# Optimization experiments

Hardware: AMD Instinct MI355X
Metric: run time of the kernel (lower is better)

Reference implementation:

```python
import jax, jax.numpy as jnp
import numpy as np
from jax import lax

B, H, W, C = 2, 256, 256, 192
HEADS = 6
WS = 8                      # window size
PW = WS // 2                # permuted window size (kv downsampled 2x2)
HIDDEN = 4 * C
HEAD_DIM = C // HEADS
SCALE = HEAD_DIM ** -0.5
N_WIN = WS * WS             # 64 query tokens per window
N_KV = PW * PW              # 16 kv tokens per window


def _aligned_index(pw0, pw1):
    ch = np.arange(pw0)
    cw = np.arange(pw1)
    coords = np.stack(np.meshgrid(ch, cw, indexing='ij'))          # (2, pw0, pw1)
    cf = coords.reshape(2, -1)
    rel = (cf[:, :, None] - cf[:, None, :]).transpose(1, 2, 0).astype(np.int64)
    rel[:, :, 0] += pw0 - 1
    rel[:, :, 1] += pw1 - 1
    rel[:, :, 0] *= 2 * pw1 - 1
    idx = rel.sum(-1)                                              # (N_KV, N_KV)
    n4 = pw0 * pw1
    idx = idx.reshape(pw0, pw1, 1, 1, n4)
    idx = np.tile(idx, (1, 1, 2, 2, 1)).transpose(0, 2, 1, 3, 4).reshape(4 * n4, n4)
    return jnp.asarray(idx)

IDX = _aligned_index(PW, PW)   # (N_WIN, N_KV)


def layernorm(x, g, b):
    mu = x.mean(-1, keepdims=True)
    var = ((x - mu) ** 2).mean(-1, keepdims=True)
    return (x - mu) * lax.rsqrt(var + 1e-5) * g + b


def window_partition(x):
    # (B, H, W, C) -> (B*nW, WS, WS, C)
    x = x.reshape(B, H // WS, WS, W // WS, WS, C)
    return x.transpose(0, 1, 3, 2, 4, 5).reshape(-1, WS, WS, C)


def window_reverse(w):
    # (B*nW, WS, WS, C) -> (B, H, W, C)
    x = w.reshape(B, H // WS, W // WS, WS, WS, C)
    return x.transpose(0, 1, 3, 2, 4, 5).reshape(B, H, W, C)


def setup_inputs() -> dict:
    key = jax.random.key(0)
    ks = jax.random.split(key, 10)
    rn = lambda k, shp, s=0.02: jax.random.normal(k, shp, jnp.float32) * s
    return {
        'x': jax.random.normal(ks[0], (B, H * W, C), jnp.float32),
        'g1': jnp.ones((C,), jnp.float32), 'be1': jnp.zeros((C,), jnp.float32),
        'wq': rn(ks[1], (C, C)), 'bq': jnp.zeros((C,), jnp.float32),
        'wkv': rn(ks[2], (C, C // 2)), 'bkv': jnp.zeros((C // 2,), jnp.float32),
        'bias_table': rn(ks[3], ((2 * PW - 1) * (2 * PW - 1), HEADS)),
        'wproj': rn(ks[4], (C, C)), 'bproj': jnp.zeros((C,), jnp.float32),
        'g2': jnp.ones((C,), jnp.float32), 'be2': jnp.zeros((C,), jnp.float32),
        'w1f': rn(ks[5], (C, HIDDEN)), 'b1f': jnp.zeros((HIDDEN,), jnp.float32),
        'dwk': rn(ks[6], (HIDDEN, 1, 5, 5)), 'dwb': jnp.zeros((HIDDEN,), jnp.float32),
        'w2f': rn(ks[7], (HIDDEN, C)), 'b2f': jnp.zeros((C,), jnp.float32),
    }


def reference(x, g1, be1, wq, bq, wkv, bkv, bias_table, wproj, bproj,
              g2, be2, w1f, b1f, dwk, dwb, w2f, b2f):
    shortcut = x
    xn = layernorm(x, g1, be1).reshape(B, H, W, C)
    xw = window_partition(xn).reshape(-1, N_WIN, C)        # (b_, 64, C)
    b_ = xw.shape[0]
    # PSA: kv downsampled 2x2 spatially, 2x2 block folded into channels
    kv = (xw @ wkv + bkv).reshape(b_, PW, 2, PW, 2, 2, C // 4)
    kv = kv.transpose(0, 1, 3, 5, 2, 4, 6).reshape(b_, N_KV, 2, HEADS, HEAD_DIM)
    kv = kv.transpose(2, 0, 3, 1, 4)                       # (2, b_, h, N_KV, d)
    k, v = kv[0], kv[1]
    q = (xw @ wq + bq).reshape(b_, N_WIN, HEADS, HEAD_DIM).transpose(0, 2, 1, 3) * SCALE
    attn = jnp.einsum('bhqd,bhkd->bhqk', q, k)             # (b_, h, 64, 16)
    bias = bias_table[IDX.reshape(-1)].reshape(N_WIN, N_KV, HEADS).transpose(2, 0, 1)
    attn = jax.nn.softmax(attn + bias[None], axis=-1)
    aw = jnp.einsum('bhqk,bhkd->bhqd', attn, v).transpose(0, 2, 1, 3).reshape(b_, N_WIN, C)
    aw = aw @ wproj + bproj
    x = shortcut + window_reverse(aw.reshape(-1, WS, WS, C)).reshape(B, H * W, C)
    # ConvFFN with depthwise-conv residual branch
    xn2 = layernorm(x, g2, be2)
    h1 = jax.nn.gelu(xn2 @ w1f + b1f, approximate=False)   # (B, HW, HIDDEN)
    img = h1.transpose(0, 2, 1).reshape(B, HIDDEN, H, W)
    conv = lax.conv_general_dilated(img, dwk, (1, 1), ((2, 2), (2, 2)),
                                    feature_group_count=HIDDEN,
                                    dimension_numbers=('NCHW', 'OIHW', 'NCHW'))
    conv = jax.nn.gelu(conv + dwb[None, :, None, None], approximate=False)
    h = h1 + conv.reshape(B, HIDDEN, H * W).transpose(0, 2, 1)
    return x + (h @ w2f + b2f)
```

## Files before the change

### kernel.cpp

```cpp
#include <hip/hip_runtime.h>
#include <hip/hip_bf16.h>
#include <math.h>

#define NTOK  131072
#define NTOKH 65536
#define CD    192
#define HID   768


typedef short bf16x8 __attribute__((ext_vector_type(8)));
typedef float f32x4  __attribute__((ext_vector_type(4)));
typedef float f32x2  __attribute__((ext_vector_type(2)));
typedef __bf16 bf16x2_t __attribute__((ext_vector_type(2)));

__device__ __forceinline__ float bf2f(unsigned short v) {
    union { unsigned int u; float f; } c; c.u = ((unsigned int)v) << 16; return c.f;
}
__device__ __forceinline__ unsigned short f2bf(float f) {
    union { float f; unsigned int u; } c; c.f = f;
    unsigned int r = c.u + 0x7FFFu + ((c.u >> 16) & 1u);
    return (unsigned short)(r >> 16);
}
__device__ __forceinline__ float lo_bf(unsigned p) {
    union { unsigned u; float f; } c; c.u = p << 16; return c.f;
}
__device__ __forceinline__ float hi_bf(unsigned p) {
    union { unsigned u; float f; } c; c.u = p & 0xFFFF0000u; return c.f;
}
__device__ __forceinline__ float dot2bf(unsigned a, unsigned b, float c) {
#if __has_builtin(__builtin_amdgcn_fdot2_f32_bf16)
    union U { unsigned u; bf16x2_t v; };
    U ua, ub; ua.u = a; ub.u = b;
    return __builtin_amdgcn_fdot2_f32_bf16(ua.v, ub.v, c, false);
#else
    return fmaf(hi_bf(a) , hi_bf(b), fmaf(lo_bf(a), lo_bf(b), c));
#endif
}
__device__ __forceinline__ float gelu_f(float x) {
    float t = x * 0.7071067811865476f;
    t = fminf(fmaxf(t, -4.0f), 4.0f);
    float s2 = t * t;
    float p = fmaf(s2, -2.72614225801306e-10f, 2.77068142495902e-08f);
    p = fmaf(s2, p, -2.10102402082508e-06f);
    p = fmaf(s2, p, -5.69250639462346e-05f);
    p = fmaf(s2, p, -7.34990630326855e-04f);
    p = fmaf(s2, p, -2.95459980854025e-03f);
    p = fmaf(s2, p, -1.60960333262415e-02f);
    p = p * t;
    float q = fmaf(s2, -1.45660718464996e-05f, -2.13374055278905e-04f);
    q = fmaf(s2, q, -1.68282697438203e-03f);
    q = fmaf(s2, q, -7.37332916720468e-03f);
    q = fmaf(s2, q, -1.42647390514189e-02f);
    float er = p * __builtin_amdgcn_rcpf(q);
    return 0.5f * x * (1.0f + er);
}

__device__ __forceinline__ void gld16(const unsigned short* g, unsigned short* l) {
    __builtin_amdgcn_global_load_lds(
        (const __attribute__((address_space(1))) void*)(unsigned long long)(g),
        (__attribute__((address_space(3))) void*)(unsigned int)(unsigned long long)(l),
        16, 0, 0);
}

__global__ __launch_bounds__(256) void ln_kernel(const float* __restrict__ x,
                                                 const float* __restrict__ g,
                                                 const float* __restrict__ b,
                                                 unsigned short* __restrict__ out) {
    int tok  = blockIdx.x * 4 + (threadIdx.x >> 6);
    int lane = threadIdx.x & 63;
    const float* xp = x + (size_t)tok * CD;
    float v0 = xp[lane], v1 = xp[lane + 64], v2 = xp[lane + 128];
    float s  = v0 + v1 + v2;
    float s2 = v0 * v0 + v1 * v1 + v2 * v2;
    #pragma unroll
    for (int off = 32; off > 0; off >>= 1) {
        s  += __shfl_xor(s,  off, 64);
        s2 += __shfl_xor(s2, off, 64);
    }
    float mu  = s * (1.0f / 192.0f);
    float var = s2 * (1.0f / 192.0f) - mu * mu;
    float rs  = rsqrtf(var + 1e-5f);
    unsigned short* op = out + (size_t)tok * CD;
    op[lane]       = f2bf((v0 - mu) * rs * g[lane]       + b[lane]);
    op[lane + 64]  = f2bf((v1 - mu) * rs * g[lane + 64]  + b[lane + 64]);
    op[lane + 128] = f2bf((v2 - mu) * rs * g[lane + 128] + b[lane + 128]);
}

__global__ __launch_bounds__(256) void wconv_kernel(
    const float* __restrict__ wq, const float* __restrict__ wkv,
    const float* __restrict__ wproj, const float* __restrict__ w1f,
    const float* __restrict__ w2f,
    unsigned short* __restrict__ qkvT, unsigned short* __restrict__ projT,
    unsigned short* __restrict__ w1T, unsigned short* __restrict__ w2T)
{
    int i = blockIdx.x * 256 + threadIdx.x;
    if (i < 288 * 192) {
        int n = i / 192, k = i - n * 192;
        float v = (n < 192) ? wq[(size_t)k * 192 + n] : wkv[(size_t)k * 96 + (n - 192)];
        qkvT[n * 192 + k] = f2bf(v);
    }
    if (i < 192 * 192) {
        int n = i / 192, k = i - n * 192;
        projT[n * 192 + k] = f2bf(wproj[(size_t)k * 192 + n]);
    }
    {
        int n = i / 192, k = i - n * 192;
        w1T[n * 192 + k] = f2bf(w1f[(size_t)k * 768 + n]);
    }
    {
        int n = i / 768, k = i - n * 768;
        w2T[n * 768 + k] = f2bf(w2f[(size_t)k * 192 + n]);
    }
}

__global__ __launch_bounds__(256) void dwprep_kernel(
    const float* __restrict__ dwk, unsigned int* __restrict__ pP, float* __restrict__ pS)
{
    int i = blockIdx.x * 256 + threadIdx.x;
    if (i >= 768 * 5) return;
    const float* w = dwk + (size_t)i * 5;
    unsigned b0 = f2bf(w[0]), b1 = f2bf(w[1]), b2 = f2bf(w[2]),
             b3 = f2bf(w[3]), b4 = f2bf(w[4]);
    pP[i * 4 + 0] = b0 | (b1 << 16);
    pP[i * 4 + 1] = b2 | (b3 << 16);
    pP[i * 4 + 2] = b1 | (b2 << 16);
    pP[i * 4 + 3] = b3 | (b4 << 16);
    pS[i * 2 + 0] = w[0];
    pS[i * 2 + 1] = w[4];
}

__device__ __forceinline__ void xcd_swz(int gx, int& bx, int& by) {
    int nwg  = gx * (int)gridDim.y;
    int id   = (int)blockIdx.y * gx + (int)blockIdx.x;
    int q    = nwg >> 3, r = nwg & 7;
    int xcd  = id & 7, rest = id >> 3;
    int sw   = (xcd < r ? xcd * (q + 1) : r * (q + 1) + (xcd - r) * q) + rest;
    bx = sw % gx; by = sw / gx;
}

template<int MODE>
__global__ __launch_bounds__(256) void mgemm_kernel(
    const unsigned short* __restrict__ A,
    const unsigned short* __restrict__ WT,
    const float* __restrict__ b0, const float* __restrict__ b1,
    const float* __restrict__ addsrc,
    void* O0, unsigned short* __restrict__ O1,
    int K, int Nreal)
{
    constexpr int BM = 128, BN = 96, BK = 64;
    __shared__ unsigned short As[BM * BK];
    __shared__ unsigned short Bs[BN * BK];
    const int tid  = threadIdx.x;
    const int wave = tid >> 6, lane = tid & 63;
    const int quad = lane >> 4, l16 = lane & 15;
    const int wm = (wave >> 1) * 64, wn = (wave & 1) * 48;
    int bx, by; xcd_swz(gridDim.x, bx, by);
    const int m0 = by * BM, n0 = bx * BN;

    f32x4 acc[4][3];
    #pragma unroll
    for (int mi = 0; mi < 4; mi++)
        #pragma unroll
        for (int ni = 0; ni < 3; ni++) acc[mi][ni] = (f32x4){0.f, 0.f, 0.f, 0.f};

    const int r8 = lane >> 3;
    const int sw = ((lane & 7) ^ r8) << 3;
    const unsigned short* aSrc = A  + (size_t)(m0 + wave * 32 + r8) * K + sw;
    const unsigned short* bSrc = WT + (size_t)(n0 + wave * 24 + r8) * K + sw;
    unsigned short* aDst = &As[(wave * 32) * BK];
    unsigned short* bDst = &Bs[(wave * 24) * BK];

    for (int k0 = 0; k0 < K; k0 += BK) {
        #pragma unroll
        for (int i = 0; i < 4; i++)
            gld16(aSrc + k0 + i * 8 * K, aDst + i * 8 * BK);
        #pragma unroll
        for (int i = 0; i < 3; i++)
            gld16(bSrc + k0 + i * 8 * K, bDst + i * 8 * BK);
        __syncthreads();

        #pragma unroll
        for (int kk = 0; kk < 2; kk++) {
            const int cb = kk * 64 + quad * 16;
            bf16x8 bfr[3];
            #pragma unroll
            for (int ni = 0; ni < 3; ni++) {
                int br = wn + ni * 16 + l16;
                bfr[ni] = *(const bf16x8*)&Bs[br * BK + ((cb ^ ((br & 7) << 4)) >> 1)];
            }
            #pragma unroll
            for (int mi = 0; mi < 4; mi++) {
                int ar = wm + mi * 16 + l16;
                bf16x8 af = *(const bf16x8*)&As[ar * BK + ((cb ^ ((ar & 7) << 4)) >> 1)];
                acc[mi][0] = __builtin_amdgcn_mfma_f32_16x16x32_bf16(af, bfr[0], acc[mi][0], 0, 0, 0);
                acc[mi][1] = __builtin_amdgcn_mfma_f32_16x16x32_bf16(af, bfr[1], acc[mi][1], 0, 0, 0);
                acc[mi][2] = __builtin_amdgcn_mfma_f32_16x16x32_bf16(af, bfr[2], acc[mi][2], 0, 0, 0);
            }
        }
        __syncthreads();
    }

    float bc[3], bc1[3];
    #pragma unroll
    for (int ni = 0; ni < 3; ni++) {
        int col = n0 + wn + ni * 16 + l16;
        if (MODE == 0) {
            if (n0 < 192) bc[ni] = b0[col];
            else          bc1[ni] = b1[col - 192];
        } else {
            bc[ni] = b0[col];
        }
    }
    #pragma unroll
    for (int mi = 0; mi < 4; mi++) {
        int row0 = m0 + wm + mi * 16 + quad * 4;
        #pragma unroll
        for (int r = 0; r < 4; r++) {
            unsigned mrow = (unsigned)(row0 + r);
            if (MODE == 0) {
                if (n0 < 192) {
                    unsigned ob = mrow * 192u + (unsigned)(n0 + wn + l16);
                    unsigned short* q0 = (unsigned short*)O0;
                    #pragma unroll
                    for (int ni = 0; ni < 3; ni++)
                        q0[ob + ni * 16] = f2bf((acc[mi][ni][r] + bc[ni]) * 0.17677669529663687f);
                } else {
                    unsigned ob = mrow * 96u + (unsigned)(n0 - 192 + wn + l16);
                    #pragma unroll
                    for (int ni = 0; ni < 3; ni++)
                        O1[ob + ni * 16] = f2bf(acc[mi][ni][r] + bc1[ni]);
                }
            } else if (MODE == 1) {
                unsigned ob = mrow * 192u + (unsigned)(n0 + wn + l16);
                float* op = (float*)O0;
                #pragma unroll
                for (int ni = 0; ni < 3; ni++)
                    op[ob + ni * 16] = acc[mi][ni][r] + bc[ni] + addsrc[ob + ni * 16];
            } else if (MODE == 2) {
                unsigned ob = mrow * 768u + (unsigned)(n0 + wn + l16);
                unsigned short* op = (unsigned short*)O0;
                #pragma unroll
                for (int ni = 0; ni < 3; ni++)
                    op[ob + ni * 16] = f2bf(gelu_f(acc[mi][ni][r] + bc[ni]));
            } else {
                unsigned ob = mrow * 192u + (unsigned)(n0 + wn + l16);
                float* op = (float*)O0;
                #pragma unroll
                for (int ni = 0; ni < 3; ni++)
                    op[ob + ni * 16] = op[ob + ni * 16] + acc[mi][ni][r] + bc[ni];
            }
        }
    }
}

__global__ __launch_bounds__(384) void attn_kernel(
    const unsigned short* __restrict__ q, const unsigned short* __restrict__ kvp,
    const float* __restrict__ bt, unsigned short* __restrict__ aw)
{
    __shared__ float ks[6][16][32];
    __shared__ float vs[6][16][32];
    const int w = blockIdx.x;
    const int b = w >> 10, rem = w & 1023, wh = rem >> 5, wc = rem & 31;
    const int tid = threadIdx.x;
    const size_t base = (size_t)b * 65536;

    for (int e = tid; e < 16 * 192; e += 384) {
        int kk = e / 192, f = e - kk * 192;
        int d1 = kk >> 2, d3 = kk & 3;
        int d2 = f / 96;  int r = f - d2 * 96;
        int d4 = r / 48;  int c4 = r - d4 * 48;
        int i = 2 * d1 + d2, j = 2 * d3 + d4;
        size_t g = base + (size_t)(wh * 8 + i) * 256 + (wc * 8 + j);
        int h = f >> 5, d = f & 31;
        ks[h][kk][d] = bf2f(kvp[g * 96 + c4]);
        vs[h][kk][d] = bf2f(kvp[g * 96 + 48 + c4]);
    }
    __syncthreads();

    const int t = tid & 63, h = tid >> 6;
    const int i = t >> 3, j = t & 7;
    const int iq2 = i >> 1, jq2 = j >> 1;
    const size_t g = base + (size_t)(wh * 8 + i) * 256 + (wc * 8 + j);

    f32x2 qr[16];
    const ushort4* qp = (const ushort4*)(q + g * 192 + h * 32);
    #pragma unroll
    for (int d4i = 0; d4i < 8; d4i++) {
        ushort4 u = qp[d4i];
        qr[d4i * 2 + 0] = (f32x2){bf2f(u.x), bf2f(u.y)};
        qr[d4i * 2 + 1] = (f32x2){bf2f(u.z), bf2f(u.w)};
    }

    float lg[16]; float mx = -1e30f;
    #pragma unroll
    for (int kk = 0; kk < 16; kk++) {
        int kh = kk >> 2, kw = kk & 3;
        const f32x2* kp = (const f32x2*)&ks[h][kk][0];
        f32x2 a2 = (f32x2){bt[((iq2 - kh + 3) * 7 + (jq2 - kw + 3)) * 6 + h], 0.f};
        #pragma unroll
        for (int d = 0; d < 16; d++) a2 = __builtin_elementwise_fma(qr[d], kp[d], a2);
        float s = a2.x + a2.y;
        lg[kk] = s; mx = fmaxf(mx, s);
    }
    float den = 0.f;
    #pragma unroll
    for (int kk = 0; kk < 16; kk++) { lg[kk] = expf(lg[kk] - mx); den += lg[kk]; }
    float inv = 1.0f / den;

    f32x2 oacc[16];
    #pragma unroll
    for (int d = 0; d < 16; d++) oacc[d] = (f32x2){0.f, 0.f};
    #pragma unroll
    for (int kk = 0; kk < 16; kk++) {
        float p = lg[kk] * inv;
        f32x2 pv = (f32x2){p, p};
        const f32x2* vp = (const f32x2*)&vs[h][kk][0];
        #pragma unroll
        for (int d = 0; d < 16; d++) oacc[d] = __builtin_elementwise_fma(pv, vp[d], oacc[d]);
    }
    unsigned int* op = (unsigned int*)(aw + g * 192 + h * 32);
    #pragma unroll
    for (int d = 0; d < 16; d++) {
        unsigned int lo = f2bf(oacc[d].x), hi = f2bf(oacc[d].y);
        op[d] = lo | (hi << 16);
    }
}

__global__ __launch_bounds__(256) void dwconv_kernel(
    const unsigned short* __restrict__ h1,
    const float* __restrict__ dwk, const float* __restrict__ dwb,
    const unsigned int* __restrict__ pP, const float* __restrict__ pS,
    unsigned short* __restrict__ hout)
{
    __shared__ unsigned short tile[12][12][64];
    int bx = blockIdx.x;
    int chb = bx % 12; int t = bx / 12;
    int tw = t % 32; int th = t / 32;
    const int tid = threadIdx.x;
    const int chbase = chb * 64;
    const int ch = tid & 63;
    const int cp = tid >> 6;
    const int c0 = cp * 2;
    const int gch = chbase + ch;
    const float bias = dwb[gch];

    const int lane4 = tid & 15;
    const int pg = tid >> 4;

#if __has_builtin(__builtin_amdgcn_fdot2_f32_bf16)
    unsigned wA[5][2], wB[5][2]; float w0s[5], w4s[5];
    #pragma unroll
    for (int kr = 0; kr < 5; kr++) {
        int idx = gch * 5 + kr;
        wA[kr][0] = pP[idx * 4 + 0];
        wA[kr][1] = pP[idx * 4 + 1];
        wB[kr][0] = pP[idx * 4 + 2];
        wB[kr][1] = pP[idx * 4 + 3];
        w0s[kr]   = pS[idx * 2 + 0];
        w4s[kr]   = pS[idx * 2 + 1];
    }
    for (int p = pg; p < 144; p += 16) {
        int pr = p / 12, pc = p - pr * 12;
        int r = th * 8 - 2 + pr, c = tw * 8 - 2 + pc;
        ushort4 u = make_ushort4(0, 0, 0, 0);
        if (r >= 0 && r < 256 && c >= 0 && c < 256)
            u = *(const ushort4*)(h1 + (((size_t)r * 256 + c) * HID + chbase + lane4 * 4));
        *(ushort4*)&tile[pr][pc][lane4 * 4] = u;
    }
    __syncthreads();

    unsigned pw[5][3];
    #pragma unroll
    for (int rr = 0; rr < 4; rr++)
        #pragma unroll
        for (int j = 0; j < 3; j++)
            pw[rr][j] = (unsigned)tile[rr][c0 + 2 * j][ch]
                      | ((unsigned)tile[rr][c0 + 2 * j + 1][ch] << 16);

    unsigned obase = ((unsigned)(th * 8) * 256u + (unsigned)(tw * 8 + c0)) * (unsigned)HID
                   + (unsigned)gch;

    #pragma unroll
    for (int r0 = 0; r0 < 8; r0++) {
        const int rn = (r0 + 4) % 5;
        #pragma unroll
        for (int j = 0; j < 3; j++)
            pw[rn][j] = (unsigned)tile[r0 + 4][c0 + 2 * j][ch]
                      | ((unsigned)tile[r0 + 4][c0 + 2 * j + 1][ch] << 16);

        float s0 = bias, s1 = bias;
        #pragma unroll
        for (int kr = 0; kr < 5; kr++) {
            const int ri = (r0 + kr) % 5;
            s0 = dot2bf(pw[ri][0], wA[kr][0], s0);
            s0 = dot2bf(pw[ri][1], wA[kr][1], s0);
            s0 = fmaf(lo_bf(pw[ri][2]), w4s[kr], s0);
            s1 = fmaf(hi_bf(pw[ri][0]), w0s[kr], s1);
            s1 = dot2bf(pw[ri][1], wB[kr][0], s1);
            s1 = dot2bf(pw[ri][2], wB[kr][1], s1);
        }
        const int rc = (r0 + 2) % 5;
        float v0 = lo_bf(pw[rc][1]) + gelu_f(s0);
        float v1 = hi_bf(pw[rc][1]) + gelu_f(s1);
        hout[obase]       = f2bf(v0);
        hout[obase + HID] = f2bf(v1);
        obase += 256u * (unsigned)HID;
    }
#else
    float w[25];
    #pragma unroll
    for (int tap = 0; tap < 25; tap++)
        w[tap] = dwk[(size_t)gch * 25 + tap];
    for (int p = pg; p < 144; p += 16) {
        int pr = p / 12, pc = p - pr * 12;
        int r = th * 8 - 2 + pr, c = tw * 8 - 2 + pc;
        ushort4 u = make_ushort4(0, 0, 0, 0);
        if (r >= 0 && r < 256 && c >= 0 && c < 256)
            u = *(const ushort4*)(h1 + (((size_t)r * 256 + c) * HID + chbase + lane4 * 4));
        *(ushort4*)&tile[pr][pc][lane4 * 4] = u;
    }
    __syncthreads();
    float win[5][6];
    #pragma unroll
    for (int rr = 0; rr < 4; rr++)
        #pragma unroll
        for (int cc = 0; cc < 6; cc++)
            win[rr][cc] = bf2f(tile[rr][c0 + cc][ch]);
    unsigned obase = ((unsigned)(th * 8) * 256u + (unsigned)(tw * 8 + c0)) * (unsigned)HID
                   + (unsigned)gch;
    #pragma unroll
    for (int r0 = 0; r0 < 8; r0++) {
        #pragma unroll
        for (int cc = 0; cc < 6; cc++)
            win[(r0 + 4) % 5][cc] = bf2f(tile[r0 + 4][c0 + cc][ch]);
        float s0 = bias, s1 = bias;
        #pragma unroll
        for (int kr = 0; kr < 5; kr++) {
            int ri = (r0 + kr) % 5;
            #pragma unroll
            for (int kc = 0; kc < 5; kc++) {
                float wt = w[kr * 5 + kc];
                s0 = fmaf(win[ri][kc],     wt, s0);
                s1 = fmaf(win[ri][kc + 1], wt, s1);
            }
        }
        const int rc = (r0 + 2) % 5;
        float v0 = win[rc][2] + gelu_f(s0);
        float v1 = win[rc][3] + gelu_f(s1);
        hout[obase]       = f2bf(v0);
        hout[obase + HID] = f2bf(v1);
        obase += 256u * (unsigned)HID;
    }
#endif
}

extern "C" void kernel_launch(void* const* d_in, const int* in_sizes, int n_in,
                              void* d_out, int out_size, void* d_ws, size_t ws_size,
                              hipStream_t stream) {
    const float* x    = (const float*)d_in[0];
    const float* g1   = (const float*)d_in[1];
    const float* be1  = (const float*)d_in[2];
    const float* wq   = (const float*)d_in[3];
    const float* bq   = (const float*)d_in[4];
    const float* wkv  = (const float*)d_in[5];
    const float* bkv  = (const float*)d_in[6];
    const float* btab = (const float*)d_in[7];
    const float* wproj= (const float*)d_in[8];
    const float* bproj= (const float*)d_in[9];
    const float* g2   = (const float*)d_in[10];
    const float* be2  = (const float*)d_in[11];
    const float* w1f  = (const float*)d_in[12];
    const float* b1f  = (const float*)d_in[13];
    const float* dwk  = (const float*)d_in[14];
    const float* dwb  = (const float*)d_in[15];
    const float* w2f  = (const float*)d_in[16];
    const float* b2f  = (const float*)d_in[17];
    float* out = (float*)d_out;

    char* ws = (char*)d_ws;
    unsigned short* xnb  = (unsigned short*)(ws);
    unsigned short* qb   = (unsigned short*)(ws + 50331648);
    unsigned short* kvb  = (unsigned short*)(ws + 100663296);
    unsigned short* h1b  = (unsigned short*)(ws + 125829120);
    unsigned short* hhb  = (unsigned short*)(ws + 226492416);
    unsigned short* qkvT = (unsigned short*)(ws + 327155712);
    unsigned short* projT= (unsigned short*)(ws + 327266304);
    unsigned short* w1T  = (unsigned short*)(ws + 327340032);
    unsigned short* w2T  = (unsigned short*)(ws + 327634944);
    unsigned int* dwpP = (unsigned int*)(ws);
    float*        dwpS = (float*)(ws + 61440);

    wconv_kernel<<<576, 256, 0, stream>>>(wq, wkv, wproj, w1f, w2f,
                                          qkvT, projT, w1T, w2T);
    ln_kernel<<<NTOK / 4, 256, 0, stream>>>(x, g1, be1, xnb);
    mgemm_kernel<0><<<dim3(3, NTOK / 128), 256, 0, stream>>>(
        xnb, qkvT, bq, bkv, nullptr, qb, kvb, 192, 288);
    attn_kernel<<<2048, 384, 0, stream>>>(qb, kvb, btab, xnb);
    mgemm_kernel<1><<<dim3(2, NTOK / 128), 256, 0, stream>>>(
        xnb, projT, bproj, nullptr, x, out, nullptr, 192, 192);
    dwprep_kernel<<<15, 256, 0, stream>>>(dwk, dwpP, dwpS);
    ln_kernel<<<NTOK / 4, 256, 0, stream>>>(out, g2, be2, qb);
    for (int half = 0; half < 2; half++) {
        const unsigned short* xn2h = qb + (size_t)half * NTOKH * CD;
        float* outh = out + (size_t)half * NTOKH * CD;
        mgemm_kernel<2><<<dim3(8, NTOKH / 128), 256, 0, stream>>>(
            xn2h, w1T, b1f, nullptr, nullptr, h1b, nullptr, 192, 768);
        dwconv_kernel<<<12 * 32 * 32, 256, 0, stream>>>(h1b, dwk, dwb, dwpP, dwpS, hhb);
        mgemm_kernel<3><<<dim3(2, NTOKH / 128), 256, 0, stream>>>(
            hhb, w2T, b2f, nullptr, nullptr, outh, nullptr, 768, 192);
    }
}
```

Baseline: 733.3 us.

## Double-buffer shared-memory tiles in the MFMA GEMM with a smaller K step

The GEMM kernel now uses two shared-memory buffers for A and B with the K tile halved to 32. The next tile is prefetched into the alternate buffer while MFMAs run on the current one, leaving one barrier per iteration instead of two. The intent is to hide global-to-LDS load latency behind matrix compute. In exchange there are twice as many K iterations, and the staging pattern is uneven, with some waves loading two B row groups and others one. The LDS swizzle is also changed to match the narrower tile.

```diff
diff --git a/kernel.cpp b/kernel.cpp
--- a/kernel.cpp
+++ b/kernel.cpp
@@ -147,9 +147,9 @@
     void* O0, unsigned short* __restrict__ O1,
     int K, int Nreal)
 {
-    constexpr int BM = 128, BN = 96, BK = 64;
-    __shared__ unsigned short As[BM * BK];
-    __shared__ unsigned short Bs[BN * BK];
+    constexpr int BM = 128, BN = 96, BK = 32;
+    __shared__ unsigned short As[2][BM * BK];
+    __shared__ unsigned short Bs[2][BN * BK];
     const int tid  = threadIdx.x;
     const int wave = tid >> 6, lane = tid & 63;
     const int quad = lane >> 4, l16 = lane & 15;
@@ -163,50 +163,63 @@
         #pragma unroll
         for (int ni = 0; ni < 3; ni++) acc[mi][ni] = (f32x4){0.f, 0.f, 0.f, 0.f};
 
-    const int r8 = lane >> 3;
-    const int sw = ((lane & 7) ^ r8) << 3;
-    const unsigned short* aSrc = A  + (size_t)(m0 + wave * 32 + r8) * K + sw;
-    const unsigned short* bSrc = WT + (size_t)(n0 + wave * 24 + r8) * K + sw;
-    unsigned short* aDst = &As[(wave * 32) * BK];
-    unsigned short* bDst = &Bs[(wave * 24) * BK];
-
-    for (int k0 = 0; k0 < K; k0 += BK) {
-        #pragma unroll
-        for (int i = 0; i < 4; i++)
-            gld16(aSrc + k0 + i * 8 * K, aDst + i * 8 * BK);
-        #pragma unroll
-        for (int i = 0; i < 3; i++)
-            gld16(bSrc + k0 + i * 8 * K, bDst + i * 8 * BK);
+    const int r16 = lane >> 2;
+    const int sw  = ((lane & 3) ^ ((r16 >> 1) & 3)) << 3;
+    const unsigned short* aS0 = A + (size_t)(m0 + wave * 32      + r16) * K + sw;
+    const unsigned short* aS1 = A + (size_t)(m0 + wave * 32 + 16 + r16) * K + sw;
+    const int bc0 = (wave < 2) ? wave * 2     : 4 + (wave - 2);
+    const int bc1 = (wave < 2) ? wave * 2 + 1 : -1;
+    const unsigned short* bS0 = WT + (size_t)(n0 + bc0 * 16 + r16) * K + sw;
+    const unsigned short* bS1 = WT + (size_t)(n0 + (bc1 < 0 ? 0 : bc1) * 16 + r16) * K + sw;
+    unsigned short* aD0 = &As[0][(wave * 32) * BK];
+    unsigned short* aD1 = &As[0][(wave * 32 + 16) * BK];
+    unsigned short* bD0 = &Bs[0][(bc0 * 16) * BK];
+    unsigned short* bD1 = &Bs[0][((bc1 < 0 ? 0 : bc1) * 16) * BK];
+    const int bufStrA = BM * BK;
+    const int bufStrB = BN * BK;
+
+    const int nt = K / BK;
+    {
+        gld16(aS0, aD0); gld16(aS1, aD1); gld16(bS0, bD0);
+        if (bc1 >= 0) gld16(bS1, bD1);
+    }
+    __syncthreads();
+
+    int cur = 0;
+    for (int t = 0; t < nt; ++t) {
+        if (t + 1 < nt) {
+            int ko = (t + 1) * BK;
+            int nb = (cur ^ 1);
+            gld16(aS0 + ko, aD0 + nb * bufStrA);
+            gld16(aS1 + ko, aD1 + nb * bufStrA);
+            gld16(bS0 + ko, bD0 + nb * bufStrB);
+            if (bc1 >= 0) gld16(bS1 + ko, bD1 + nb * bufStrB);
+        }
+        bf16x8 bfr[3];
+        #pragma unroll
+        for (int ni = 0; ni < 3; ni++) {
+            int br = wn + ni * 16 + l16;
+            bfr[ni] = *(const bf16x8*)&Bs[cur][br * BK + ((quad ^ ((br >> 1) & 3)) << 3)];
+        }
+        #pragma unroll
+        for (int mi = 0; mi < 4; mi++) {
+            int ar = wm + mi * 16 + l16;
+            bf16x8 af = *(const bf16x8*)&As[cur][ar * BK + ((quad ^ ((ar >> 1) & 3)) << 3)];
+            acc[mi][0] = __builtin_amdgcn_mfma_f32_16x16x32_bf16(af, bfr[0], acc[mi][0], 0, 0, 0);
+            acc[mi][1] = __builtin_amdgcn_mfma_f32_16x16x32_bf16(af, bfr[1], acc[mi][1], 0, 0, 0);
+            acc[mi][2] = __builtin_amdgcn_mfma_f32_16x16x32_bf16(af, bfr[2], acc[mi][2], 0, 0, 0);
+        }
         __syncthreads();
-
-        #pragma unroll
-        for (int kk = 0; kk < 2; kk++) {
-            const int cb = kk * 64 + quad * 16;
-            bf16x8 bfr[3];
-            #pragma unroll
-            for (int ni = 0; ni < 3; ni++) {
-                int br = wn + ni * 16 + l16;
-                bfr[ni] = *(const bf16x8*)&Bs[br * BK + ((cb ^ ((br & 7) << 4)) >> 1)];
-            }
-            #pragma unroll
-            for (int mi = 0; mi < 4; mi++) {
-                int ar = wm + mi * 16 + l16;
-                bf16x8 af = *(const bf16x8*)&As[ar * BK + ((cb ^ ((ar & 7) << 4)) >> 1)];
-                acc[mi][0] = __builtin_amdgcn_mfma_f32_16x16x32_bf16(af, bfr[0], acc[mi][0], 0, 0, 0);
-                acc[mi][1] = __builtin_amdgcn_mfma_f32_16x16x32_bf16(af, bfr[1], acc[mi][1], 0, 0, 0);
-                acc[mi][2] = __builtin_amdgcn_mfma_f32_16x16x32_bf16(af, bfr[2], acc[mi][2], 0, 0, 0);
-            }
-        }
-        __syncthreads();
-    }
-
-    float bc[3], bc1[3];
+        cur ^= 1;
+    }
+
+    float bc[3], bcc1[3];
     #pragma unroll
     for (int ni = 0; ni < 3; ni++) {
         int col = n0 + wn + ni * 16 + l16;
         if (MODE == 0) {
             if (n0 < 192) bc[ni] = b0[col];
-            else          bc1[ni] = b1[col - 192];
+            else          bcc1[ni] = b1[col - 192];
         } else {
             bc[ni] = b0[col];
         }
@@ -228,7 +241,7 @@
                     unsigned ob = mrow * 96u + (unsigned)(n0 - 192 + wn + l16);
                     #pragma unroll
                     for (int ni = 0; ni < 3; ni++)
-                        O1[ob + ni * 16] = f2bf(acc[mi][ni][r] + bc1[ni]);
+                        O1[ob + ni * 16] = f2bf(acc[mi][ni][r] + bcc1[ni]);
                 }
             } else if (MODE == 1) {
                 unsigned ob = mrow * 192u + (unsigned)(n0 + wn + l16);
```

Result: slower. 752.5 us (+2.6%).
